# Optimization experiments

Hardware: AMD Instinct MI355X
Metric: run time of the kernel (lower is better)

The kernel has to match this reference:

```python
import jax, jax.numpy as jnp
import numpy as np

NUM_BASES = 5
STRIDE = (1, 1)
PADDING = ((1, 1), (1, 1))
DN = ('NCHW', 'OIHW', 'NCHW')


def quantize_act(x):
    # Q_A_DOREFA forward: round(clamp(x, 0, 1)) -> values in {0, 1}
    return jnp.round(jnp.clip(x, 0.0, 1.0))


def quantize_w(w):
    # Q_W forward: sign(w) * mean(|w|) over the whole weight tensor of one basis
    return jnp.sign(w) * jnp.mean(jnp.abs(w))


def setup_inputs() -> dict:
    key = jax.random.key(0)
    kx, kw = jax.random.split(key)
    x = jax.random.normal(kx, (8, 256, 64, 64), dtype=jnp.float32)
    # 5 bases, each an OIHW conv kernel [256, 256, 3, 3]
    weights = jax.random.normal(kw, (NUM_BASES, 256, 256, 3, 3), dtype=jnp.float32) * 0.05
    return {"x": x, "weights": weights}


def reference(x, weights):
    xq = quantize_act(x)
    # quantize each basis independently (per-basis scalar scale)
    wq = jax.vmap(quantize_w)(weights)  # [5, O, I, kh, kw]
    # conv is linear in the kernel: sum of 5 convs == conv with summed kernels
    w_sum = jnp.sum(wq, axis=0)
    out = jax.lax.conv_general_dilated(
        xq, w_sum, window_strides=STRIDE, padding=PADDING,
        dimension_numbers=DN)
    return out / NUM_BASES
```

## Files before the change

### kernel.cpp

```cpp
#include <hip/hip_runtime.h>
#include <hip/hip_bf16.h>

typedef __attribute__((ext_vector_type(4))) int i32x4;

constexpr int NB = 8, CI = 256, OC = 256, HH = 64, WW = 64, HP = 66, WP = 66;
constexpr int NBASES = 5;
constexpr int WELEMS = OC * CI * 9;
constexpr int NT = 36;

__global__ void k_abs_partial(const float* __restrict__ w, float* __restrict__ part) {
    int b = blockIdx.x >> 6, chunk = blockIdx.x & 63;
    const float4* v = (const float4*)(w + (size_t)b * WELEMS + (size_t)chunk * (WELEMS / 64));
    float s = 0.f;
    for (int i = threadIdx.x; i < WELEMS / 64 / 4; i += 256) {
        float4 t = v[i];
        s += fabsf(t.x) + fabsf(t.y) + fabsf(t.z) + fabsf(t.w);
    }
    #pragma unroll
    for (int off = 32; off; off >>= 1) s += __shfl_down(s, off, 64);
    __shared__ float ls[4];
    int lane = threadIdx.x & 63, wid = threadIdx.x >> 6;
    if (lane == 0) ls[wid] = s;
    __syncthreads();
    if (threadIdx.x == 0) part[blockIdx.x] = ls[0] + ls[1] + ls[2] + ls[3];
}

__global__ void k_prep(const float* __restrict__ w, const float* __restrict__ part,
                       signed char* __restrict__ wsum8, float* __restrict__ scl,
                       const float* __restrict__ x, signed char* __restrict__ xq) {
    __shared__ float sLDS[NBASES];
    int tid = threadIdx.x;

    if (blockIdx.x < OC) {
        if (tid < 64) {
            #pragma unroll
            for (int b = 0; b < NBASES; ++b) {
                float v = part[b * 64 + tid];
                #pragma unroll
                for (int off = 32; off; off >>= 1) v += __shfl_down(v, off, 64);
                if (tid == 0) sLDS[b] = v * (1.0f / (float)WELEMS);
            }
        }
        __syncthreads();
        float sc[NBASES];
        #pragma unroll
        for (int b = 0; b < NBASES; ++b) sc[b] = sLDS[b];
        float sSum = sc[0] + sc[1] + sc[2] + sc[3] + sc[4];
        float invS = 127.0f / sSum;
        if (blockIdx.x == 0 && tid == 0)
            scl[0] = sSum * (0.2f / 127.0f);

        int o = blockIdx.x, i = tid;
        const float* base = w + ((size_t)(o * CI + i)) * 9;
        float acc[9];
        #pragma unroll
        for (int t = 0; t < 9; ++t) acc[t] = 0.f;
        #pragma unroll
        for (int b = 0; b < NBASES; ++b) {
            const float* wb = base + (size_t)b * WELEMS;
            #pragma unroll
            for (int t = 0; t < 9; ++t) {
                float xv = wb[t];
                acc[t] += (xv > 0.f) ? sc[b] : ((xv < 0.f) ? -sc[b] : 0.f);
            }
        }
        #pragma unroll
        for (int t = 0; t < 9; ++t)
            wsum8[(t * OC + o) * CI + i] = (signed char)__float2int_rn(acc[t] * invS);
        return;
    }

    int nh = blockIdx.x - OC, n = nh >> 6, h = nh & 63;
    const float* xb = x + ((size_t)n * CI) * (HH * WW) + h * WW;
    signed char* ob = xq + ((size_t)(n * HP + (h + 1)) * WP + 1) * CI;
    int w4 = tid >> 2;
    int cl = tid & 3;
    #pragma unroll
    for (int p = 0; p < 4; ++p) {
        int c = (p * 4 + cl) * 16;
        signed char pk[16];
        #pragma unroll
        for (int i = 0; i < 16; ++i) {
            float v = xb[(size_t)(c + i) * (HH * WW) + w4];
            pk[i] = (signed char)rintf(fminf(fmaxf(v, 0.f), 1.f));
        }
        *(int4*)(ob + w4 * CI + c) = *(const int4*)pk;
    }
    (ob - CI)[tid] = 0;
    (ob + 64 * CI)[tid] = 0;
    if (h == 0) {
        signed char* r0 = xq + ((size_t)(n * HP + 0) * WP) * CI;
        int4 z = {0, 0, 0, 0};
        for (int i = tid; i < WP * CI / 16; i += 256) *(int4*)(r0 + i * 16) = z;
    }
    if (h == HH - 1) {
        signed char* r65 = xq + ((size_t)(n * HP + (HP - 1)) * WP) * CI;
        int4 z = {0, 0, 0, 0};
        for (int i = tid; i < WP * CI / 16; i += 256) *(int4*)(r65 + i * 16) = z;
    }
}

__launch_bounds__(256, 2)
__global__ void k_conv(const signed char* __restrict__ xq,
                       const signed char* __restrict__ wsum,
                       const float* __restrict__ scl,
                       float* __restrict__ out) {
    __shared__ __align__(16) signed char lA[4][128 * 64];
    __shared__ __align__(16) signed char lB[4][128 * 64];

    float so = scl[0];

    int bid = blockIdx.x;
    int bx = ((bid & 7) << 6) | (bid >> 3);
    int pt = bx >> 1, ot = bx & 1;
    int pb = pt * 128;
    int n = pb >> 12;
    int h0 = (pb >> 6) & 63;
    int oc0 = ot * 128;
    int tid = threadIdx.x;

    int base0 = (n * HP + h0) * WP * CI;
    int bBase0 = oc0 * CI;

    int aOff[2], bOff[2];
    #pragma unroll
    for (int k = 0; k < 2; ++k) {
        int c = tid + k * 256;
        int row = c >> 2, sp = c & 3;
        int l = sp ^ ((row >> 1) & 3);
        aOff[k] = ((row >> 6) * WP + (row & 63)) * CI + l * 16;
        bOff[k] = row * CI + l * 16;
    }

    int lane = tid & 63, wid = tid >> 6;
    int wm = wid >> 1, wn = wid & 1;
    int g = lane >> 4, r16 = lane & 15;
    int fA[4], fB[4];
    #pragma unroll
    for (int q = 0; q < 4; ++q) {
        int ra = wm * 64 + q * 16 + r16;
        fA[q] = ra * 64 + (g ^ ((ra >> 1) & 3)) * 16;
        int rb = wn * 64 + q * 16 + r16;
        fB[q] = rb * 64 + (g ^ ((rb >> 1) & 3)) * 16;
    }

    i32x4 acc[4][4] = {};

    auto stage = [&](int t) {
        int buf = t & 3;
        int tap = t >> 2;
        int c0 = (t & 3) << 6;
        int kh = (tap * 171) >> 9;
        int kw = tap - kh * 3;
        const signed char* aSrc = xq + base0 + (kh * WP + kw) * CI + c0;
        const signed char* bSrc = wsum + tap * (OC * CI) + bBase0 + c0;
        #pragma unroll
        for (int k = 0; k < 2; ++k) {
            __builtin_amdgcn_global_load_lds(
                (const __attribute__((address_space(1))) void*)(aSrc + aOff[k]),
                (__attribute__((address_space(3))) void*)(&lA[buf][(tid + k * 256) * 16]), 16, 0, 0);
            __builtin_amdgcn_global_load_lds(
                (const __attribute__((address_space(1))) void*)(bSrc + bOff[k]),
                (__attribute__((address_space(3))) void*)(&lB[buf][(tid + k * 256) * 16]), 16, 0, 0);
        }
    };

    stage(0); stage(1); stage(2);

    #pragma unroll 1
    for (int t = 0; t < NT; ++t) {
        int buf = t & 3;
        if (t <= NT - 3)      asm volatile("s_waitcnt vmcnt(8)" ::: "memory");
        else if (t == NT - 2) asm volatile("s_waitcnt vmcnt(4)" ::: "memory");
        else                  asm volatile("s_waitcnt vmcnt(0)" ::: "memory");
        __builtin_amdgcn_s_barrier();
        __builtin_amdgcn_sched_barrier(0);
        if (t + 3 < NT) stage(t + 3);

        i32x4 aR[4], bR[4];
        #pragma unroll
        for (int q = 0; q < 4; ++q) aR[q] = *(const i32x4*)&lA[buf][fA[q]];
        #pragma unroll
        for (int q = 0; q < 4; ++q) bR[q] = *(const i32x4*)&lB[buf][fB[q]];
        __builtin_amdgcn_s_setprio(1);
        #pragma unroll
        for (int mq = 0; mq < 4; ++mq)
            #pragma unroll
            for (int nq = 0; nq < 4; ++nq)
                acc[mq][nq] = __builtin_amdgcn_mfma_i32_16x16x64_i8(
                    aR[mq], bR[nq], acc[mq][nq], 0, 0, 0);
        __builtin_amdgcn_s_setprio(0);
    }

    int hw0 = pb & 4095;
    #pragma unroll
    for (int mq = 0; mq < 4; ++mq) {
        int pl = wm * 64 + mq * 16 + g * 4;
        #pragma unroll
        for (int nq = 0; nq < 4; ++nq) {
            int oc = oc0 + wn * 64 + nq * 16 + r16;
            float4 v;
            v.x = (float)acc[mq][nq][0] * so;
            v.y = (float)acc[mq][nq][1] * so;
            v.z = (float)acc[mq][nq][2] * so;
            v.w = (float)acc[mq][nq][3] * so;
            *(float4*)(out + ((size_t)(n * OC + oc) << 12) + hw0 + pl) = v;
        }
    }
}

extern "C" void kernel_launch(void* const* d_in, const int* in_sizes, int n_in,
                              void* d_out, int out_size, void* d_ws, size_t ws_size,
                              hipStream_t stream) {
    (void)in_sizes; (void)n_in; (void)out_size; (void)ws_size;
    const float* x   = (const float*)d_in[0];
    const float* wts = (const float*)d_in[1];
    float* out = (float*)d_out;
    char* wsb = (char*)d_ws;
    float* part          = (float*)wsb;
    float* scl           = (float*)(wsb + 2048);
    signed char* wsum8   = (signed char*)(wsb + 4096);
    signed char* xq8     = (signed char*)(wsb + (size_t)(2u << 20));

    hipLaunchKernelGGL(k_abs_partial, dim3(NBASES * 64), dim3(256), 0, stream, wts, part);
    hipLaunchKernelGGL(k_prep, dim3(OC + NB * HH), dim3(256), 0, stream,
                       wts, part, wsum8, scl, x, xq8);
    hipLaunchKernelGGL(k_conv, dim3((NB * HH * WW / 128) * (OC / 128)), dim3(256), 0, stream,
                       xq8, wsum8, scl, out);
}
```

Measured before the change: 53.82 us.

## Double-buffer LDS fragments in registers to overlap reads with MFMA

Restructures the conv main loop so the LDS fragments for the next K-step are loaded into a second register set while the MFMA cluster runs on the current one. The loop is unrolled by two and alternates between the two register sets, and the wait counts are adjusted for the new ordering. This aims to hide LDS read latency behind the matrix ops. In exchange it raises register pressure, which could hurt occupancy under launch_bounds(256,2), and the tighter wait and barrier sequencing is harder to keep correct.

Measured after the change: 52.75 us. 2.0% less time.

```diff
diff --git a/kernel.cpp b/kernel.cpp
--- a/kernel.cpp
+++ b/kernel.cpp
@@ -164,24 +164,13 @@
                 (__attribute__((address_space(3))) void*)(&lB[buf][(tid + k * 256) * 16]), 16, 0, 0);
         }
     };
-
-    stage(0); stage(1); stage(2);
-
-    #pragma unroll 1
-    for (int t = 0; t < NT; ++t) {
-        int buf = t & 3;
-        if (t <= NT - 3)      asm volatile("s_waitcnt vmcnt(8)" ::: "memory");
-        else if (t == NT - 2) asm volatile("s_waitcnt vmcnt(4)" ::: "memory");
-        else                  asm volatile("s_waitcnt vmcnt(0)" ::: "memory");
-        __builtin_amdgcn_s_barrier();
-        __builtin_amdgcn_sched_barrier(0);
-        if (t + 3 < NT) stage(t + 3);
-
-        i32x4 aR[4], bR[4];
+    auto readFrags = [&](int buf, i32x4 (&aR)[4], i32x4 (&bR)[4]) {
         #pragma unroll
         for (int q = 0; q < 4; ++q) aR[q] = *(const i32x4*)&lA[buf][fA[q]];
         #pragma unroll
         for (int q = 0; q < 4; ++q) bR[q] = *(const i32x4*)&lB[buf][fB[q]];
+    };
+    auto mfmaCluster = [&](i32x4 (&aR)[4], i32x4 (&bR)[4]) {
         __builtin_amdgcn_s_setprio(1);
         #pragma unroll
         for (int mq = 0; mq < 4; ++mq)
@@ -190,6 +179,40 @@
                 acc[mq][nq] = __builtin_amdgcn_mfma_i32_16x16x64_i8(
                     aR[mq], bR[nq], acc[mq][nq], 0, 0, 0);
         __builtin_amdgcn_s_setprio(0);
+    };
+
+    stage(0); stage(1); stage(2);
+    asm volatile("s_waitcnt vmcnt(8)" ::: "memory");
+    __builtin_amdgcn_s_barrier();
+    i32x4 a0[4], b0[4], a1[4], b1[4];
+    readFrags(0, a0, b0);
+
+    #pragma unroll 1
+    for (int p = 0; p < NT / 2; ++p) {
+        int t = 2 * p;
+        {
+            if (t + 2 <= NT - 1) asm volatile("s_waitcnt vmcnt(4)" ::: "memory");
+            else                 asm volatile("s_waitcnt vmcnt(0)" ::: "memory");
+            __builtin_amdgcn_s_barrier();
+            __builtin_amdgcn_sched_barrier(0);
+            if (t + 3 < NT) stage(t + 3);
+            readFrags((t + 1) & 3, a1, b1);
+            __builtin_amdgcn_sched_barrier(0);
+            mfmaCluster(a0, b0);
+        }
+        t = 2 * p + 1;
+        {
+            if (t < NT - 1) {
+                if (t + 2 <= NT - 1) asm volatile("s_waitcnt vmcnt(4)" ::: "memory");
+                else                 asm volatile("s_waitcnt vmcnt(0)" ::: "memory");
+                __builtin_amdgcn_s_barrier();
+                __builtin_amdgcn_sched_barrier(0);
+                if (t + 3 < NT) stage(t + 3);
+                readFrags((t + 1) & 3, a0, b0);
+                __builtin_amdgcn_sched_barrier(0);
+            }
+            mfmaCluster(a1, b1);
+        }
     }
 
     int hw0 = pb & 4095;
```

## Load MFMA fragments directly from global memory, dropping LDS staging

Applied to the files above, without the earlier changes.

Replaces the 4-stage LDS pipeline (global_load_lds plus barriers) with direct per-wave global loads into registers, double-buffered across even and odd k-steps. This removes the barrier synchronisation and LDS traffic and frees shared memory. In exchange, tiles shared between waves are fetched redundantly from global or L2, and the prefetch distance shrinks to one step, which exposes memory latency.

New measurement: 92.59 us. +72.0%, slower.

```diff
diff --git a/kernel.cpp b/kernel.cpp
--- a/kernel.cpp
+++ b/kernel.cpp
@@ -105,11 +105,6 @@
                        const signed char* __restrict__ wsum,
                        const float* __restrict__ scl,
                        float* __restrict__ out) {
-    __shared__ __align__(16) signed char lA[4][128 * 64];
-    __shared__ __align__(16) signed char lB[4][128 * 64];
-
-    float so = scl[0];
-
     int bid = blockIdx.x;
     int bx = ((bid & 7) << 6) | (bid >> 3);
     int pt = bx >> 1, ot = bx & 1;
@@ -120,68 +115,44 @@
     int tid = threadIdx.x;
 
     int base0 = (n * HP + h0) * WP * CI;
-    int bBase0 = oc0 * CI;
-
-    int aOff[2], bOff[2];
-    #pragma unroll
-    for (int k = 0; k < 2; ++k) {
-        int c = tid + k * 256;
-        int row = c >> 2, sp = c & 3;
-        int l = sp ^ ((row >> 1) & 3);
-        aOff[k] = ((row >> 6) * WP + (row & 63)) * CI + l * 16;
-        bOff[k] = row * CI + l * 16;
-    }
 
     int lane = tid & 63, wid = tid >> 6;
     int wm = wid >> 1, wn = wid & 1;
     int g = lane >> 4, r16 = lane & 15;
-    int fA[4], fB[4];
+
+    int pA[4];
     #pragma unroll
     for (int q = 0; q < 4; ++q) {
         int ra = wm * 64 + q * 16 + r16;
-        fA[q] = ra * 64 + (g ^ ((ra >> 1) & 3)) * 16;
-        int rb = wn * 64 + q * 16 + r16;
-        fB[q] = rb * 64 + (g ^ ((rb >> 1) & 3)) * 16;
+        pA[q] = ((ra >> 6) * WP + (ra & 63)) * CI + g * 16;
+    }
+    int pB[4];
+    #pragma unroll
+    for (int q = 0; q < 4; ++q) {
+        int rb = oc0 + wn * 64 + q * 16 + r16;
+        pB[q] = rb * CI + g * 16;
     }
 
     i32x4 acc[4][4] = {};
 
-    auto stage = [&](int t) {
-        int buf = t & 3;
+    auto tapBaseA = [&](int t) {
         int tap = t >> 2;
         int c0 = (t & 3) << 6;
         int kh = (tap * 171) >> 9;
         int kw = tap - kh * 3;
-        const signed char* aSrc = xq + base0 + (kh * WP + kw) * CI + c0;
-        const signed char* bSrc = wsum + tap * (OC * CI) + bBase0 + c0;
-        #pragma unroll
-        for (int k = 0; k < 2; ++k) {
-            __builtin_amdgcn_global_load_lds(
-                (const __attribute__((address_space(1))) void*)(aSrc + aOff[k]),
-                (__attribute__((address_space(3))) void*)(&lA[buf][(tid + k * 256) * 16]), 16, 0, 0);
-            __builtin_amdgcn_global_load_lds(
-                (const __attribute__((address_space(1))) void*)(bSrc + bOff[k]),
-                (__attribute__((address_space(3))) void*)(&lB[buf][(tid + k * 256) * 16]), 16, 0, 0);
-        }
-    };
-
-    stage(0); stage(1); stage(2);
-
-    #pragma unroll 1
-    for (int t = 0; t < NT; ++t) {
-        int buf = t & 3;
-        if (t <= NT - 3)      asm volatile("s_waitcnt vmcnt(8)" ::: "memory");
-        else if (t == NT - 2) asm volatile("s_waitcnt vmcnt(4)" ::: "memory");
-        else                  asm volatile("s_waitcnt vmcnt(0)" ::: "memory");
-        __builtin_amdgcn_s_barrier();
-        __builtin_amdgcn_sched_barrier(0);
-        if (t + 3 < NT) stage(t + 3);
-
-        i32x4 aR[4], bR[4];
-        #pragma unroll
-        for (int q = 0; q < 4; ++q) aR[q] = *(const i32x4*)&lA[buf][fA[q]];
-        #pragma unroll
-        for (int q = 0; q < 4; ++q) bR[q] = *(const i32x4*)&lB[buf][fB[q]];
+        return base0 + (kh * WP + kw) * CI + c0;
+    };
+    auto loadA = [&](int t, i32x4 (&aR)[4]) {
+        const signed char* s = xq + tapBaseA(t);
+        #pragma unroll
+        for (int q = 0; q < 4; ++q) aR[q] = *(const i32x4*)(s + pA[q]);
+    };
+    auto loadB = [&](int t, i32x4 (&bR)[4]) {
+        const signed char* s = wsum + (t >> 2) * (OC * CI) + ((t & 3) << 6);
+        #pragma unroll
+        for (int q = 0; q < 4; ++q) bR[q] = *(const i32x4*)(s + pB[q]);
+    };
+    auto mfmaCluster = [&](i32x4 (&aR)[4], i32x4 (&bR)[4]) {
         __builtin_amdgcn_s_setprio(1);
         #pragma unroll
         for (int mq = 0; mq < 4; ++mq)
@@ -190,8 +161,21 @@
                 acc[mq][nq] = __builtin_amdgcn_mfma_i32_16x16x64_i8(
                     aR[mq], bR[nq], acc[mq][nq], 0, 0, 0);
         __builtin_amdgcn_s_setprio(0);
-    }
-
+    };
+
+    i32x4 aE[4], bE[4], aO[4], bO[4];
+    loadA(0, aE); loadB(0, bE);
+    #pragma unroll 1
+    for (int p = 0; p < NT / 2; ++p) {
+        int t = 2 * p;
+        if (t + 1 < NT) { loadA(t + 1, aO); loadB(t + 1, bO); }
+        mfmaCluster(aE, bE);
+        t = 2 * p + 1;
+        if (t + 1 < NT) { loadA(t + 1, aE); loadB(t + 1, bE); }
+        mfmaCluster(aO, bO);
+    }
+
+    float so = scl[0];
     int hw0 = pb & 4095;
     #pragma unroll
     for (int mq = 0; mq < 4; ++mq) {
```
